# Optimization experiments

Hardware: AMD Instinct MI355X
Metric: run time of the kernel (lower is better)

Reference implementation:

```python
import jax, jax.numpy as jnp
import numpy as np

B, S, H, N = 2, 2048, 1024, 16
D = H // N


def setup_inputs() -> dict:
    key = jax.random.key(0)
    k1, k2, k3 = jax.random.split(key, 3)
    # Xavier-uniform-ish init for projection weights
    lim_in = (6.0 / (H + 3 * H)) ** 0.5
    lim_out = (6.0 / (H + H)) ** 0.5
    return {
        "hidden_states": jax.random.normal(k1, (B, S, H), dtype=jnp.float32),
        "w_in": jax.random.uniform(k2, (3 * H, H), minval=-lim_in, maxval=lim_in, dtype=jnp.float32),
        "b_in": jnp.zeros((3 * H,), dtype=jnp.float32),
        "w_out": jax.random.uniform(k3, (H, H), minval=-lim_out, maxval=lim_out, dtype=jnp.float32),
        "b_out": jnp.zeros((H,), dtype=jnp.float32),
    }


def reference(hidden_states, w_in, b_in, w_out, b_out):
    b, s, h = hidden_states.shape
    qkv = hidden_states @ w_in.T + b_in  # [B,S,3H]
    q, k, v = jnp.split(qkv, 3, axis=-1)
    # [B,S,H] -> [B,N,S,D]
    def to_heads(x):
        return x.reshape(b, s, N, D).transpose(0, 2, 1, 3)
    q, k, v = to_heads(q), to_heads(k), to_heads(v)
    scale = D ** -0.5
    scores = jnp.einsum("bnqd,bnkd->bnqk", q, k) * scale  # [B,N,S,S]
    causal = jnp.triu(jnp.ones((s, s), dtype=bool), k=1)
    scores = jnp.where(causal, -jnp.inf, scores)
    attn = jax.nn.softmax(scores, axis=-1)
    out = jnp.einsum("bnqk,bnkd->bnqd", attn, v)  # [B,N,S,D]
    out = out.transpose(0, 2, 1, 3).reshape(b, s, h)
    return out @ w_out.T + b_out
```

## Files before the change

kernel.cpp:

```cpp
#include <hip/hip_runtime.h>
#include <hip/hip_bf16.h>

#define BB 2
#define SS 2048
#define HH 1024
#define NH 16
#define DD 64
#define H3 3072
#define MM (BB*SS)

typedef unsigned short u16;
typedef unsigned int u32;
typedef __attribute__((ext_vector_type(8))) short bf16x8;
typedef __attribute__((ext_vector_type(4))) float f32x4;

__device__ __forceinline__ u16 f2bf(float f) {
    union { float f; u32 u; } v; v.f = f;
    u32 u = v.u;
    u += 0x7fffu + ((u >> 16) & 1u);
    return (u16)(u >> 16);
}
__device__ __forceinline__ float bf2f(u16 h) {
    union { u32 u; float f; } v; v.u = ((u32)h) << 16;
    return v.f;
}
__device__ __forceinline__ u32 pack2bf(float a, float b) {
    __hip_bfloat162 h = __float22bfloat162_rn(float2{a, b});
    u32 u; __builtin_memcpy(&u, &h, 4);
    return u;
}
__device__ __forceinline__ void gl_lds16(const void* g, void* l) {
    __builtin_amdgcn_global_load_lds(
        (const __attribute__((address_space(1))) u32*)g,
        (__attribute__((address_space(3))) u32*)l, 16, 0, 0);
}
__device__ __forceinline__ int ginv(int R) {
    return (R & 35) | ((R & 8) << 1) | ((R & 4) << 1) | ((R & 16) >> 2);
}

__global__ void cvt3bf(const float4* __restrict__ s0, uint2* __restrict__ d0, int n0,
                       const float4* __restrict__ s1, uint2* __restrict__ d1, int n1,
                       const float4* __restrict__ s2, uint2* __restrict__ d2, int n2) {
    int i = blockIdx.x * blockDim.x + threadIdx.x;
    const int tot = n0 + n1 + n2;
    for (; i < tot; i += gridDim.x * blockDim.x) {
        const float4* s; uint2* d; int j;
        if (i < n0)            { s = s0; d = d0; j = i; }
        else if (i < n0 + n1)  { s = s1; d = d1; j = i - n0; }
        else                   { s = s2; d = d2; j = i - n0 - n1; }
        float4 v = s[j];
        uint2 o; o.x = pack2bf(v.x, v.y); o.y = pack2bf(v.z, v.w);
        d[j] = o;
    }
}

template<int BN, int MODE>
__global__ __launch_bounds__(256, 3)
void gemm_k2(const u16* __restrict__ A, const u16* __restrict__ Bbf,
             const u16* __restrict__ biasbf, void* __restrict__ Cptr,
             u16* __restrict__ Qo, u16* __restrict__ Ko, u16* __restrict__ Vto,
             int M, int Nn, int K)
{
    constexpr int NFR = BN / 32;
    __shared__ __align__(16) u16 Alds[2][128 * 32];
    __shared__ __align__(16) u16 Blds[2][BN * 32];
    const int tid = threadIdx.x;
    const int w = tid >> 6, lane = tid & 63, quad = lane >> 4, l16 = lane & 15;
    const int m0 = blockIdx.x * 128, n0 = blockIdx.y * BN;
    const int wm = w >> 1, wn = w & 1;
    const int rA4 = lane >> 2, c8b = (lane & 3) * 8;

    f32x4 acc[4][NFR] = {};

#define GSTAGE(k0_, bi_) do {                                                  \
    _Pragma("unroll")                                                          \
    for (int q = 0; q < 2; ++q) {                                              \
        int row0 = w * 32 + q * 16;                                            \
        gl_lds16(&A[(size_t)(m0 + row0 + rA4) * K + (k0_) + c8b],              \
                 &Alds[bi_][row0 * 32]);                                       \
    }                                                                          \
    _Pragma("unroll")                                                          \
    for (int q = 0; q < BN / 64; ++q) {                                        \
        int row0 = w * (BN / 4) + q * 16;                                      \
        gl_lds16(&Bbf[(size_t)(n0 + row0 + rA4) * K + (k0_) + c8b],            \
                 &Blds[bi_][row0 * 32]);                                       \
    }                                                                          \
} while (0)

    const int NT = K >> 5;
    GSTAGE(0, 0);
    for (int t = 0; t < NT; ++t) {
        const int cur = t & 1;
        __syncthreads();
        if (t + 1 < NT) GSTAGE((t + 1) << 5, cur ^ 1);

        bf16x8 af[4], bfr[NFR];
#pragma unroll
        for (int mi = 0; mi < 4; ++mi)
            af[mi] = *(const bf16x8*)&Alds[cur][(wm * 64 + mi * 16 + l16) * 32 + quad * 8];
#pragma unroll
        for (int ni = 0; ni < NFR; ++ni)
            bfr[ni] = *(const bf16x8*)&Blds[cur][(wn * (BN / 2) + ni * 16 + l16) * 32 + quad * 8];
#pragma unroll
        for (int mi = 0; mi < 4; ++mi)
#pragma unroll
            for (int ni = 0; ni < NFR; ++ni)
                acc[mi][ni] = __builtin_amdgcn_mfma_f32_16x16x32_bf16(
                    af[mi], bfr[ni], acc[mi][ni], 0, 0, 0);
    }
#undef GSTAGE

#pragma unroll
    for (int mi = 0; mi < 4; ++mi) {
        int row_b = m0 + wm * 64 + mi * 16 + quad * 4;
#pragma unroll
        for (int ni = 0; ni < NFR; ++ni) {
            int col = n0 + wn * (BN / 2) + ni * 16 + l16;
            float bv = bf2f(biasbf[col]);
            if constexpr (MODE == 1) {
#pragma unroll
                for (int i = 0; i < 4; ++i)
                    ((float*)Cptr)[(size_t)(row_b + i) * Nn + col] = acc[mi][ni][i] + bv;
            } else {
                if (col < 1024) {
#pragma unroll
                    for (int i = 0; i < 4; ++i)
                        Qo[(size_t)(row_b + i) * 1024 + col] =
                            f2bf((acc[mi][ni][i] + bv) * 0.125f);
                } else if (col < 2048) {
#pragma unroll
                    for (int i = 0; i < 4; ++i)
                        Ko[(size_t)(row_b + i) * 1024 + (col - 1024)] =
                            f2bf(acc[mi][ni][i] + bv);
                } else {
                    int d = col - 2048, hh = d >> 6, dd = d & 63;
                    int b = row_b >> 11, s = row_b & 2047;
                    u16 t0 = f2bf(acc[mi][ni][0] + bv), t1 = f2bf(acc[mi][ni][1] + bv);
                    u16 t2 = f2bf(acc[mi][ni][2] + bv), t3 = f2bf(acc[mi][ni][3] + bv);
                    uint2 pk; pk.x = (u32)t0 | ((u32)t1 << 16);
                    pk.y = (u32)t2 | ((u32)t3 << 16);
                    *(uint2*)&Vto[((size_t)((b * 16 + hh) * 64 + dd)) * 2048 + s] = pk;
                }
            }
        }
    }
}

__global__ __launch_bounds__(256, 1)
void attn_v6(const u16* __restrict__ Q, const u16* __restrict__ Kb,
             const u16* __restrict__ Vt, u16* __restrict__ attn_out) {
    const int bid = blockIdx.x;
    const int r8 = bid & 7, qq = bid >> 3;
    const int pr = qq & 7, g = (qq >> 3) * 8 + r8;
    const int h = g & 15, b = g >> 4;
    const int tid = threadIdx.x;
    const int w = tid >> 6, lane = tid & 63, quad = lane >> 4, l16 = lane & 15;
    __shared__ __align__(16) u16 Klds[2][64 * 64];
    __shared__ __align__(16) u16 Vlds[2][64 * 64];

    const int sl = lane >> 3, cch = lane & 7;
    const int rho0 = (2 * w) * 8 + sl, rho1 = (2 * w + 1) * 8 + sl;
    const int gcs = (cch ^ sl) * 8;
    const int kg0 = ginv(rho0), kg1 = ginv(rho1);
    const int ls0 = (2 * w) * 512, ls1 = (2 * w + 1) * 512;
    const int xk0 = (quad ^ (l16 & 7)) * 8;
    const int xk1 = ((quad + 4) ^ (l16 & 7)) * 8;
    const int thr = w * 16 + l16;

    const u16* Kg = Kb + (size_t)(b * SS) * 1024 + h * 64;
    const u16* Vg = Vt + (size_t)((b * 16 + h) * 64) * 2048;

#define STAGE_T(kv0_, bi_) do {                                               \
        gl_lds16(&Kg[(size_t)((kv0_) + kg0) * 1024 + gcs], &Klds[bi_][ls0]);  \
        gl_lds16(&Kg[(size_t)((kv0_) + kg1) * 1024 + gcs], &Klds[bi_][ls1]);  \
        gl_lds16(&Vg[(size_t)rho0 * 2048 + (kv0_) + gcs], &Vlds[bi_][ls0]);   \
        gl_lds16(&Vg[(size_t)rho1 * 2048 + (kv0_) + gcs], &Vlds[bi_][ls1]);   \
    } while (0)

#define ATTN_TILE(t_, MA_, MB_) do {                                          \
    const int cur_ = (t_) & 1;                                                \
    __syncthreads();   \
    if ((t_) + 1 < T) STAGE_T(((t_) + 1) * 64, cur_ ^ 1);                     \
    const u16* Kc_ = Klds[cur_];                                              \
    const u16* Vc_ = Vlds[cur_];                                              \
    f32x4 sA[4] = {}; f32x4 sB[4] = {};                                       \
    _Pragma("unroll")                                                         \
    for (int ni = 0; ni < 4; ++ni) {                                          \
        const int rb = (ni * 16 + l16) * 64;                                  \
        bf16x8 kf0 = *(const bf16x8*)&Kc_[rb + xk0];                          \
        bf16x8 kf1 = *(const bf16x8*)&Kc_[rb + xk1];                          \
        if ((MA_) != 2) {                                                     \
            sA[ni] = __builtin_amdgcn_mfma_f32_16x16x32_bf16(kf0, qfA0, sA[ni], 0, 0, 0); \
            sA[ni] = __builtin_amdgcn_mfma_f32_16x16x32_bf16(kf1, qfA1, sA[ni], 0, 0, 0); \
        }                                                                     \
        sB[ni] = __builtin_amdgcn_mfma_f32_16x16x32_bf16(kf0, qfB0, sB[ni], 0, 0, 0); \
        sB[ni] = __builtin_amdgcn_mfma_f32_16x16x32_bf16(kf1, qfB1, sB[ni], 0, 0, 0); \
    }                                                                         \
    u32 pkA[4][2], pkB[4][2];                                                 \
    _Pragma("unroll")                                                         \
    for (int ni = 0; ni < 4; ++ni) {                                          \
        const int pb = 32 * (ni >> 1) + 8 * quad + 4 * (ni & 1);              \
        if ((MA_) == 0) {                                                     \
            float p0 = __expf(sA[ni][0]), p1 = __expf(sA[ni][1]);             \
            float p2 = __expf(sA[ni][2]), p3 = __expf(sA[ni][3]);             \
            lpA += (p0 + p1) + (p2 + p3);                                     \
            pkA[ni][0] = pack2bf(p0, p1); pkA[ni][1] = pack2bf(p2, p3);       \
        } else if ((MA_) == 1) {                                              \
            float pv[4];                                                      \
            _Pragma("unroll")                                                 \
            for (int i = 0; i < 4; ++i) {                                     \
                float e = __expf(sA[ni][i]);                                  \
                pv[i] = (pb + i <= thr) ? e : 0.f;                            \
            }                                                                 \
            lpA += (pv[0] + pv[1]) + (pv[2] + pv[3]);                         \
            pkA[ni][0] = pack2bf(pv[0], pv[1]); pkA[ni][1] = pack2bf(pv[2], pv[3]); \
        }                                                                     \
        if ((MB_) == 0) {                                                     \
            float p0 = __expf(sB[ni][0]), p1 = __expf(sB[ni][1]);             \
            float p2 = __expf(sB[ni][2]), p3 = __expf(sB[ni][3]);             \
            lpB += (p0 + p1) + (p2 + p3);                                     \
            pkB[ni][0] = pack2bf(p0, p1); pkB[ni][1] = pack2bf(p2, p3);       \
        } else {                                                              \
            float pv[4];                                                      \
            _Pragma("unroll")                                                 \
            for (int i = 0; i < 4; ++i) {                                     \
                float e = __expf(sB[ni][i]);                                  \
                pv[i] = (pb + i <= thr) ? e : 0.f;                            \
            }                                                                 \
            lpB += (pv[0] + pv[1]) + (pv[2] + pv[3]);                         \
            pkB[ni][0] = pack2bf(pv[0], pv[1]); pkB[ni][1] = pack2bf(pv[2], pv[3]); \
        }                                                                     \
    }                                                                         \
    union { u32 u[4]; bf16x8 v; } pA0, pA1, pB0, pB1;                         \
    pA0.u[0] = pkA[0][0]; pA0.u[1] = pkA[0][1];                               \
    pA0.u[2] = pkA[1][0]; pA0.u[3] = pkA[1][1];                               \
    pA1.u[0] = pkA[2][0]; pA1.u[1] = pkA[2][1];                               \
    pA1.u[2] = pkA[3][0]; pA1.u[3] = pkA[3][1];                               \
    pB0.u[0] = pkB[0][0]; pB0.u[1] = pkB[0][1];                               \
    pB0.u[2] = pkB[1][0]; pB0.u[3] = pkB[1][1];                               \
    pB1.u[0] = pkB[2][0]; pB1.u[1] = pkB[2][1];                               \
    pB1.u[2] = pkB[3][0]; pB1.u[3] = pkB[3][1];                               \
    _Pragma("unroll")                                                         \
    for (int ni = 0; ni < 4; ++ni) {                                          \
        const int rb = (ni * 16 + l16) * 64;                                  \
        bf16x8 vf0 = *(const bf16x8*)&Vc_[rb + xk0];                          \
        bf16x8 vf1 = *(const bf16x8*)&Vc_[rb + xk1];                          \
        if ((MA_) != 2) {                                                     \
            oaccA[ni] = __builtin_amdgcn_mfma_f32_16x16x32_bf16(pA0.v, vf0, oaccA[ni], 0, 0, 0); \
            oaccA[ni] = __builtin_amdgcn_mfma_f32_16x16x32_bf16(pA1.v, vf1, oaccA[ni], 0, 0, 0); \
        }                                                                     \
        oaccB[ni] = __builtin_amdgcn_mfma_f32_16x16x32_bf16(pB0.v, vf0, oaccB[ni], 0, 0, 0); \
        oaccB[ni] = __builtin_amdgcn_mfma_f32_16x16x32_bf16(pB1.v, vf1, oaccB[ni], 0, 0, 0); \
    }                                                                         \
} while (0)

    for (int half = 0; half < 2; ++half) {
        const int st = half ? pr : (15 - pr);
        const int Q0 = st * 128;
        const int u2 = 2 * st;
        const int T = u2 + 2;

        const u16* Qb = Q + (size_t)(b * SS + Q0) * 1024 + h * 64;
        bf16x8 qfA0 = *(const bf16x8*)&Qb[(size_t)(w * 16 + l16) * 1024 + quad * 8];
        bf16x8 qfA1 = *(const bf16x8*)&Qb[(size_t)(w * 16 + l16) * 1024 + 32 + quad * 8];
        bf16x8 qfB0 = *(const bf16x8*)&Qb[(size_t)(64 + w * 16 + l16) * 1024 + quad * 8];
        bf16x8 qfB1 = *(const bf16x8*)&Qb[(size_t)(64 + w * 16 + l16) * 1024 + 32 + quad * 8];

        f32x4 oaccA[4] = {}, oaccB[4] = {};
        float lpA = 0.f, lpB = 0.f;

        __syncthreads();
        STAGE_T(0, 0);

        for (int t = 0; t < u2; ++t) ATTN_TILE(t, 0, 0);
        ATTN_TILE(u2, 1, 0);
        ATTN_TILE(u2 + 1, 2, 1);

        lpA += __shfl_xor(lpA, 16, 64);
        lpA += __shfl_xor(lpA, 32, 64);
        lpB += __shfl_xor(lpB, 16, 64);
        lpB += __shfl_xor(lpB, 32, 64);
        float linvA[4], linvB[4];
#pragma unroll
        for (int i = 0; i < 4; ++i) {
            linvA[i] = 1.0f / __shfl(lpA, quad * 4 + i, 64);
            linvB[i] = 1.0f / __shfl(lpB, quad * 4 + i, 64);
        }
        u16* obA = attn_out + (size_t)(b * SS + Q0 + w * 16) * 1024 + h * 64;
        u16* obB = obA + (size_t)64 * 1024;
#pragma unroll
        for (int ni = 0; ni < 4; ++ni)
#pragma unroll
            for (int i = 0; i < 4; ++i) {
                obA[(size_t)(quad * 4 + i) * 1024 + ni * 16 + l16] =
                    f2bf(oaccA[ni][i] * linvA[i]);
                obB[(size_t)(quad * 4 + i) * 1024 + ni * 16 + l16] =
                    f2bf(oaccB[ni][i] * linvB[i]);
            }
    }
#undef ATTN_TILE
#undef STAGE_T
}

extern "C" void kernel_launch(void* const* d_in, const int* in_sizes, int n_in,
                              void* d_out, int out_size, void* d_ws, size_t ws_size,
                              hipStream_t stream) {
    const float* hidden = (const float*)d_in[0];
    const float* w_in   = (const float*)d_in[1];
    const float* b_in   = (const float*)d_in[2];
    const float* w_out  = (const float*)d_in[3];
    const float* b_out  = (const float*)d_in[4];
    float* out = (float*)d_out;

    char* ws = (char*)d_ws;
    u16* hid_bf  = (u16*)d_out;
    u16* wi_bf   = (u16*)ws;
    u16* bi_bf   = (u16*)(ws + 6291456);
    u16* attn_ws = (u16*)ws;
    u16* Qbuf    = (u16*)(ws + 8388608);
    u16* wo_bf   = (u16*)(ws + 8388608);
    u16* bo_bf   = (u16*)(ws + 8388608 + 2097152);
    u16* Kbuf    = (u16*)(ws + 16777216);
    u16* Vtbuf   = (u16*)(ws + 25165824);

    cvt3bf<<<dim3(2048), dim3(256), 0, stream>>>(
        (const float4*)hidden, (uint2*)hid_bf, 1048576,
        (const float4*)w_in,   (uint2*)wi_bf,  786432,
        (const float4*)b_in,   (uint2*)bi_bf,  768);
    gemm_k2<128, 2><<<dim3(32, 24), dim3(256), 0, stream>>>(
        hid_bf, wi_bf, bi_bf, nullptr, Qbuf, Kbuf, Vtbuf, MM, H3, HH);
    attn_v6<<<dim3(256), dim3(256), 0, stream>>>(
        Qbuf, Kbuf, Vtbuf, attn_ws);
    cvt3bf<<<dim3(512), dim3(256), 0, stream>>>(
        (const float4*)w_out, (uint2*)wo_bf, 262144,
        (const float4*)b_out, (uint2*)bo_bf, 256,
        nullptr, nullptr, 0);
    gemm_k2<64, 1><<<dim3(32, 16), dim3(256), 0, stream>>>(
        attn_ws, wo_bf, bo_bf, out, nullptr, nullptr, nullptr, MM, HH, HH);
}
```

Baseline: 186.0 us.

## Split attention into 1024 smaller 64-query blocks of two waves

The attention kernel now launches 1024 blocks of 128 threads, each handling one 64-row query tile, instead of 256 blocks of 256 threads that each process two paired 128-row tiles. Each wave still computes 32 query rows (two 16-row halves). Heavy tiles are ordered first for some groups to balance the causal workload, and launch bounds now allow two blocks per CU. The aim is finer-grained scheduling and better occupancy on 256 CUs. In exchange, each block has only two waves to issue the K/V staging loads, and the number of K/V tile loads per query row goes up.

```diff
diff --git a/kernel.cpp b/kernel.cpp
--- a/kernel.cpp
+++ b/kernel.cpp
@@ -146,38 +146,50 @@
     }
 }
 
-__global__ __launch_bounds__(256, 1)
-void attn_v6(const u16* __restrict__ Q, const u16* __restrict__ Kb,
+__global__ __launch_bounds__(128, 2)
+void attn_v7(const u16* __restrict__ Q, const u16* __restrict__ Kb,
              const u16* __restrict__ Vt, u16* __restrict__ attn_out) {
     const int bid = blockIdx.x;
-    const int r8 = bid & 7, qq = bid >> 3;
-    const int pr = qq & 7, g = (qq >> 3) * 8 + r8;
+    const int r8 = bid & 7, idx = bid >> 3;
+    const int g8 = idx >> 5, m = idx & 31;
+    const int g = g8 * 8 + r8;
     const int h = g & 15, b = g >> 4;
+    const int qt = (g8 < 2) ? (31 - m) : m;
     const int tid = threadIdx.x;
     const int w = tid >> 6, lane = tid & 63, quad = lane >> 4, l16 = lane & 15;
     __shared__ __align__(16) u16 Klds[2][64 * 64];
     __shared__ __align__(16) u16 Vlds[2][64 * 64];
 
     const int sl = lane >> 3, cch = lane & 7;
-    const int rho0 = (2 * w) * 8 + sl, rho1 = (2 * w + 1) * 8 + sl;
     const int gcs = (cch ^ sl) * 8;
-    const int kg0 = ginv(rho0), kg1 = ginv(rho1);
-    const int ls0 = (2 * w) * 512, ls1 = (2 * w + 1) * 512;
+    int rho[4], kg[4], ls[4];
+#pragma unroll
+    for (int j = 0; j < 4; ++j) {
+        rho[j] = (4 * w + j) * 8 + sl;
+        kg[j]  = ginv(rho[j]);
+        ls[j]  = (4 * w + j) * 512;
+    }
     const int xk0 = (quad ^ (l16 & 7)) * 8;
     const int xk1 = ((quad + 4) ^ (l16 & 7)) * 8;
-    const int thr = w * 16 + l16;
+    const int thrA = w * 16 + l16;
+    const int thrB = 32 + w * 16 + l16;
+
+    const int Q0 = qt * 64;
+    const int T = qt + 1;
 
     const u16* Kg = Kb + (size_t)(b * SS) * 1024 + h * 64;
     const u16* Vg = Vt + (size_t)((b * 16 + h) * 64) * 2048;
+    const u16* Qb = Q  + (size_t)(b * SS + Q0) * 1024 + h * 64;
 
 #define STAGE_T(kv0_, bi_) do {                                               \
-        gl_lds16(&Kg[(size_t)((kv0_) + kg0) * 1024 + gcs], &Klds[bi_][ls0]);  \
-        gl_lds16(&Kg[(size_t)((kv0_) + kg1) * 1024 + gcs], &Klds[bi_][ls1]);  \
-        gl_lds16(&Vg[(size_t)rho0 * 2048 + (kv0_) + gcs], &Vlds[bi_][ls0]);   \
-        gl_lds16(&Vg[(size_t)rho1 * 2048 + (kv0_) + gcs], &Vlds[bi_][ls1]);   \
-    } while (0)
-
-#define ATTN_TILE(t_, MA_, MB_) do {                                          \
+    _Pragma("unroll")                                                         \
+    for (int j = 0; j < 4; ++j) {                                             \
+        gl_lds16(&Kg[(size_t)((kv0_) + kg[j]) * 1024 + gcs], &Klds[bi_][ls[j]]); \
+        gl_lds16(&Vg[(size_t)rho[j] * 2048 + (kv0_) + gcs], &Vlds[bi_][ls[j]]);  \
+    }                                                                         \
+} while (0)
+
+#define ATTN_TILE(t_, MD_) do {                                               \
     const int cur_ = (t_) & 1;                                                \
     __syncthreads();   \
     if ((t_) + 1 < T) STAGE_T(((t_) + 1) * 64, cur_ ^ 1);                     \
@@ -189,10 +201,8 @@
         const int rb = (ni * 16 + l16) * 64;                                  \
         bf16x8 kf0 = *(const bf16x8*)&Kc_[rb + xk0];                          \
         bf16x8 kf1 = *(const bf16x8*)&Kc_[rb + xk1];                          \
-        if ((MA_) != 2) {                                                     \
-            sA[ni] = __builtin_amdgcn_mfma_f32_16x16x32_bf16(kf0, qfA0, sA[ni], 0, 0, 0); \
-            sA[ni] = __builtin_amdgcn_mfma_f32_16x16x32_bf16(kf1, qfA1, sA[ni], 0, 0, 0); \
-        }                                                                     \
+        sA[ni] = __builtin_amdgcn_mfma_f32_16x16x32_bf16(kf0, qfA0, sA[ni], 0, 0, 0); \
+        sA[ni] = __builtin_amdgcn_mfma_f32_16x16x32_bf16(kf1, qfA1, sA[ni], 0, 0, 0); \
         sB[ni] = __builtin_amdgcn_mfma_f32_16x16x32_bf16(kf0, qfB0, sB[ni], 0, 0, 0); \
         sB[ni] = __builtin_amdgcn_mfma_f32_16x16x32_bf16(kf1, qfB1, sB[ni], 0, 0, 0); \
     }                                                                         \
@@ -200,35 +210,28 @@
     _Pragma("unroll")                                                         \
     for (int ni = 0; ni < 4; ++ni) {                                          \
         const int pb = 32 * (ni >> 1) + 8 * quad + 4 * (ni & 1);              \
-        if ((MA_) == 0) {                                                     \
-            float p0 = __expf(sA[ni][0]), p1 = __expf(sA[ni][1]);             \
-            float p2 = __expf(sA[ni][2]), p3 = __expf(sA[ni][3]);             \
-            lpA += (p0 + p1) + (p2 + p3);                                     \
-            pkA[ni][0] = pack2bf(p0, p1); pkA[ni][1] = pack2bf(p2, p3);       \
-        } else if ((MA_) == 1) {                                              \
-            float pv[4];                                                      \
+        if ((MD_) == 0) {                                                     \
+            float a0 = __expf(sA[ni][0]), a1 = __expf(sA[ni][1]);             \
+            float a2 = __expf(sA[ni][2]), a3 = __expf(sA[ni][3]);             \
+            lpA += (a0 + a1) + (a2 + a3);                                     \
+            pkA[ni][0] = pack2bf(a0, a1); pkA[ni][1] = pack2bf(a2, a3);       \
+            float b0 = __expf(sB[ni][0]), b1 = __expf(sB[ni][1]);             \
+            float b2 = __expf(sB[ni][2]), b3 = __expf(sB[ni][3]);             \
+            lpB += (b0 + b1) + (b2 + b3);                                     \
+            pkB[ni][0] = pack2bf(b0, b1); pkB[ni][1] = pack2bf(b2, b3);       \
+        } else {                                                              \
+            float av[4], bv4[4];                                              \
             _Pragma("unroll")                                                 \
             for (int i = 0; i < 4; ++i) {                                     \
-                float e = __expf(sA[ni][i]);                                  \
-                pv[i] = (pb + i <= thr) ? e : 0.f;                            \
+                float ea = __expf(sA[ni][i]);                                 \
+                av[i] = (pb + i <= thrA) ? ea : 0.f;                          \
+                float eb = __expf(sB[ni][i]);                                 \
+                bv4[i] = (pb + i <= thrB) ? eb : 0.f;                         \
             }                                                                 \
-            lpA += (pv[0] + pv[1]) + (pv[2] + pv[3]);                         \
-            pkA[ni][0] = pack2bf(pv[0], pv[1]); pkA[ni][1] = pack2bf(pv[2], pv[3]); \
-        }                                                                     \
-        if ((MB_) == 0) {                                                     \
-            float p0 = __expf(sB[ni][0]), p1 = __expf(sB[ni][1]);             \
-            float p2 = __expf(sB[ni][2]), p3 = __expf(sB[ni][3]);             \
-            lpB += (p0 + p1) + (p2 + p3);                                     \
-            pkB[ni][0] = pack2bf(p0, p1); pkB[ni][1] = pack2bf(p2, p3);       \
-        } else {                                                              \
-            float pv[4];                                                      \
-            _Pragma("unroll")                                                 \
-            for (int i = 0; i < 4; ++i) {                                     \
-                float e = __expf(sB[ni][i]);                                  \
-                pv[i] = (pb + i <= thr) ? e : 0.f;                            \
-            }                                                                 \
-            lpB += (pv[0] + pv[1]) + (pv[2] + pv[3]);                         \
-            pkB[ni][0] = pack2bf(pv[0], pv[1]); pkB[ni][1] = pack2bf(pv[2], pv[3]); \
+            lpA += (av[0] + av[1]) + (av[2] + av[3]);                         \
+            pkA[ni][0] = pack2bf(av[0], av[1]); pkA[ni][1] = pack2bf(av[2], av[3]); \
+            lpB += (bv4[0] + bv4[1]) + (bv4[2] + bv4[3]);                     \
+            pkB[ni][0] = pack2bf(bv4[0], bv4[1]); pkB[ni][1] = pack2bf(bv4[2], bv4[3]); \
         }                                                                     \
     }                                                                         \
     union { u32 u[4]; bf16x8 v; } pA0, pA1, pB0, pB1;                         \
@@ -245,59 +248,47 @@
         const int rb = (ni * 16 + l16) * 64;                                  \
         bf16x8 vf0 = *(const bf16x8*)&Vc_[rb + xk0];                          \
         bf16x8 vf1 = *(const bf16x8*)&Vc_[rb + xk1];                          \
-        if ((MA_) != 2) {                                                     \
-            oaccA[ni] = __builtin_amdgcn_mfma_f32_16x16x32_bf16(pA0.v, vf0, oaccA[ni], 0, 0, 0); \
-            oaccA[ni] = __builtin_amdgcn_mfma_f32_16x16x32_bf16(pA1.v, vf1, oaccA[ni], 0, 0, 0); \
-        }                                                                     \
+        oaccA[ni] = __builtin_amdgcn_mfma_f32_16x16x32_bf16(pA0.v, vf0, oaccA[ni], 0, 0, 0); \
+        oaccA[ni] = __builtin_amdgcn_mfma_f32_16x16x32_bf16(pA1.v, vf1, oaccA[ni], 0, 0, 0); \
         oaccB[ni] = __builtin_amdgcn_mfma_f32_16x16x32_bf16(pB0.v, vf0, oaccB[ni], 0, 0, 0); \
         oaccB[ni] = __builtin_amdgcn_mfma_f32_16x16x32_bf16(pB1.v, vf1, oaccB[ni], 0, 0, 0); \
     }                                                                         \
 } while (0)
 
-    for (int half = 0; half < 2; ++half) {
-        const int st = half ? pr : (15 - pr);
-        const int Q0 = st * 128;
-        const int u2 = 2 * st;
-        const int T = u2 + 2;
-
-        const u16* Qb = Q + (size_t)(b * SS + Q0) * 1024 + h * 64;
-        bf16x8 qfA0 = *(const bf16x8*)&Qb[(size_t)(w * 16 + l16) * 1024 + quad * 8];
-        bf16x8 qfA1 = *(const bf16x8*)&Qb[(size_t)(w * 16 + l16) * 1024 + 32 + quad * 8];
-        bf16x8 qfB0 = *(const bf16x8*)&Qb[(size_t)(64 + w * 16 + l16) * 1024 + quad * 8];
-        bf16x8 qfB1 = *(const bf16x8*)&Qb[(size_t)(64 + w * 16 + l16) * 1024 + 32 + quad * 8];
-
-        f32x4 oaccA[4] = {}, oaccB[4] = {};
-        float lpA = 0.f, lpB = 0.f;
-
-        __syncthreads();
-        STAGE_T(0, 0);
-
-        for (int t = 0; t < u2; ++t) ATTN_TILE(t, 0, 0);
-        ATTN_TILE(u2, 1, 0);
-        ATTN_TILE(u2 + 1, 2, 1);
-
-        lpA += __shfl_xor(lpA, 16, 64);
-        lpA += __shfl_xor(lpA, 32, 64);
-        lpB += __shfl_xor(lpB, 16, 64);
-        lpB += __shfl_xor(lpB, 32, 64);
-        float linvA[4], linvB[4];
+    bf16x8 qfA0 = *(const bf16x8*)&Qb[(size_t)(w * 16 + l16) * 1024 + quad * 8];
+    bf16x8 qfA1 = *(const bf16x8*)&Qb[(size_t)(w * 16 + l16) * 1024 + 32 + quad * 8];
+    bf16x8 qfB0 = *(const bf16x8*)&Qb[(size_t)(32 + w * 16 + l16) * 1024 + quad * 8];
+    bf16x8 qfB1 = *(const bf16x8*)&Qb[(size_t)(32 + w * 16 + l16) * 1024 + 32 + quad * 8];
+
+    f32x4 oaccA[4] = {}, oaccB[4] = {};
+    float lpA = 0.f, lpB = 0.f;
+
+    STAGE_T(0, 0);
+
+    for (int t = 0; t < T - 1; ++t) ATTN_TILE(t, 0);
+    ATTN_TILE(T - 1, 1);
+
+    lpA += __shfl_xor(lpA, 16, 64);
+    lpA += __shfl_xor(lpA, 32, 64);
+    lpB += __shfl_xor(lpB, 16, 64);
+    lpB += __shfl_xor(lpB, 32, 64);
+    float linvA[4], linvB[4];
+#pragma unroll
+    for (int i = 0; i < 4; ++i) {
+        linvA[i] = 1.0f / __shfl(lpA, quad * 4 + i, 64);
+        linvB[i] = 1.0f / __shfl(lpB, quad * 4 + i, 64);
+    }
+    u16* obA = attn_out + (size_t)(b * SS + Q0 + w * 16) * 1024 + h * 64;
+    u16* obB = obA + (size_t)32 * 1024;
+#pragma unroll
+    for (int ni = 0; ni < 4; ++ni)
 #pragma unroll
         for (int i = 0; i < 4; ++i) {
-            linvA[i] = 1.0f / __shfl(lpA, quad * 4 + i, 64);
-            linvB[i] = 1.0f / __shfl(lpB, quad * 4 + i, 64);
+            obA[(size_t)(quad * 4 + i) * 1024 + ni * 16 + l16] =
+                f2bf(oaccA[ni][i] * linvA[i]);
+            obB[(size_t)(quad * 4 + i) * 1024 + ni * 16 + l16] =
+                f2bf(oaccB[ni][i] * linvB[i]);
         }
-        u16* obA = attn_out + (size_t)(b * SS + Q0 + w * 16) * 1024 + h * 64;
-        u16* obB = obA + (size_t)64 * 1024;
-#pragma unroll
-        for (int ni = 0; ni < 4; ++ni)
-#pragma unroll
-            for (int i = 0; i < 4; ++i) {
-                obA[(size_t)(quad * 4 + i) * 1024 + ni * 16 + l16] =
-                    f2bf(oaccA[ni][i] * linvA[i]);
-                obB[(size_t)(quad * 4 + i) * 1024 + ni * 16 + l16] =
-                    f2bf(oaccB[ni][i] * linvB[i]);
-            }
-    }
 #undef ATTN_TILE
 #undef STAGE_T
 }
@@ -329,7 +320,7 @@
         (const float4*)b_in,   (uint2*)bi_bf,  768);
     gemm_k2<128, 2><<<dim3(32, 24), dim3(256), 0, stream>>>(
         hid_bf, wi_bf, bi_bf, nullptr, Qbuf, Kbuf, Vtbuf, MM, H3, HH);
-    attn_v6<<<dim3(256), dim3(256), 0, stream>>>(
+    attn_v7<<<dim3(1024), dim3(128), 0, stream>>>(
         Qbuf, Kbuf, Vtbuf, attn_ws);
     cvt3bf<<<dim3(512), dim3(256), 0, stream>>>(
         (const float4*)w_out, (uint2*)wo_bf, 262144,
```

Result: no change. 186.0 us (+0.0%).
